# Kernel optimization log

Hardware: AMD Instinct MI355X
Metric: run time of the kernel (lower is better)

Reference implementation:

```python
import jax, jax.numpy as jnp
import numpy as np

N, E, D, T = 10000, 320000, 128, 128


def _layer_norm(x, g, b, eps=1e-5):
    mu = jnp.mean(x, axis=-1, keepdims=True)
    var = jnp.mean(jnp.square(x - mu), axis=-1, keepdims=True)
    return (x - mu) * jax.lax.rsqrt(var + eps) * g + b


def setup_inputs() -> dict:
    key = jax.random.key(0)
    ks = jax.random.split(key, 24)
    s = 0.05

    def lin(k, fin, fout):
        k1, k2 = jax.random.split(k)
        return (jax.random.normal(k1, (fin, fout), jnp.float32) * s,
                jax.random.normal(k2, (fout,), jnp.float32) * s)

    W_tp, b_tp = lin(ks[5], T, D)
    W_sg, b_sg = lin(ks[6], D, D)
    W_dg, b_dg = lin(ks[7], D, D)
    W_eg, b_eg = lin(ks[8], D, D)
    W_su, b_su = lin(ks[9], D, D)
    W_du, b_du = lin(ks[10], D, D)
    return {
        'node_feats': jax.random.normal(ks[0], (N, D), jnp.float32),
        'edge_feats': jax.random.normal(ks[1], (E, D), jnp.float32),
        'time_feats': jax.random.normal(ks[2], (N, T), jnp.float32),
        'src': jax.random.randint(ks[3], (E,), 0, N),
        'dst': jax.random.randint(ks[4], (E,), 0, N),
        'W_tp': W_tp, 'b_tp': b_tp,
        'W_sg': W_sg, 'b_sg': b_sg,
        'W_dg': W_dg, 'b_dg': b_dg,
        'W_eg': W_eg, 'b_eg': b_eg,
        'W_su': W_su, 'b_su': b_su,
        'W_du': W_du, 'b_du': b_du,
        'ln_e_g': jnp.ones((D,), jnp.float32), 'ln_e_b': jnp.zeros((D,), jnp.float32),
        'ln_n_g': jnp.ones((D,), jnp.float32), 'ln_n_b': jnp.zeros((D,), jnp.float32),
    }


def reference(node_feats, edge_feats, time_feats, src, dst,
              W_tp, b_tp, W_sg, b_sg, W_dg, b_dg, W_eg, b_eg,
              W_su, b_su, W_du, b_du, ln_e_g, ln_e_b, ln_n_g, ln_n_b):
    n_nodes = node_feats.shape[0]
    # per-node gate projections (time proj folded into source gate)
    e_src = node_feats @ W_sg + b_sg + time_feats @ W_tp + b_tp   # [N, D]
    e_dst = node_feats @ W_dg + b_dg                              # [N, D]
    # edge gating: gather from both endpoints + edge feature projection
    m = e_src[src] + e_dst[dst] + edge_feats @ W_eg + b_eg        # [E, D]
    sigma = jax.nn.sigmoid(m)                                     # [E, D]
    # gated message passing: scatter-add over destination nodes
    Bh = node_feats @ W_du + b_du                                 # [N, D]
    sum_sigma_h = jax.ops.segment_sum(Bh[src] * sigma, dst, num_segments=n_nodes)
    sum_sigma = jax.ops.segment_sum(sigma, dst, num_segments=n_nodes)
    h = sum_sigma_h / (sum_sigma + 1e-6)                          # [N, D]
    x = node_feats @ W_su + b_su + h
    x = jax.nn.silu(_layer_norm(x, ln_n_g, ln_n_b))
    y = jax.nn.silu(_layer_norm(m, ln_e_g, ln_e_b))
    x = node_feats + x  # residual
    y = edge_feats + y
    return (x, y)
```

## Files before the change

### kernel.cpp

```cpp
#include <hip/hip_runtime.h>
#include <hip/hip_bf16.h>

#define N_NODES 10000
#define N_EDGES 320000
#define D 128
#define NBINS 10000

typedef float f32x4 __attribute__((ext_vector_type(4)));
typedef float f32x2 __attribute__((ext_vector_type(2)));
typedef short bf16x8 __attribute__((ext_vector_type(8)));
typedef short bf16x16 __attribute__((ext_vector_type(16)));

static __device__ inline short f2bf(float f) {
    union { __hip_bfloat16 h; short s; } u;
    u.h = __float2bfloat16(f);
    return u.s;
}

static __device__ inline float bf2f(short s) {
    union { float f; unsigned u; } x;
    x.u = ((unsigned)(unsigned short)s) << 16;
    return x.f;
}

static __device__ inline float fast_rcp(float x) { return __builtin_amdgcn_rcpf(x); }

__global__ void prep_hist(const float* __restrict__ W_sg, const float* __restrict__ W_tp,
                          const float* __restrict__ W_dg, const float* __restrict__ W_du,
                          const float* __restrict__ W_su, const float* __restrict__ W_eg,
                          short* __restrict__ Wsrc, short* __restrict__ Wdg,
                          short* __restrict__ Wdu, short* __restrict__ Wsu,
                          short* __restrict__ Weg,
                          const int* __restrict__ dst, int* __restrict__ cnt) {
    int bid = blockIdx.x;
    if (bid < 1250) {
        int i = bid * 256 + threadIdx.x;
        atomicAdd(&cnt[dst[i]], 1);
        return;
    }
    int idx = (bid - 1250) * 256 + threadIdx.x;
    const float* W0; const float* W1; short* out; int i2;
    if (idx < 32768)      { W0 = W_sg; W1 = W_tp; out = Wsrc; i2 = idx; }
    else if (idx < 49152) { W0 = W_dg; W1 = W_dg; out = Wdg;  i2 = idx - 32768; }
    else if (idx < 65536) { W0 = W_du; W1 = W_du; out = Wdu;  i2 = idx - 49152; }
    else if (idx < 81920) { W0 = W_su; W1 = W_su; out = Wsu;  i2 = idx - 65536; }
    else                  { W0 = W_eg; W1 = W_eg; out = Weg;  i2 = idx - 81920; }
    int b  = i2 & 7;
    int l  = (i2 >> 3) & 63;
    int jt = (i2 >> 9) & 7;
    int t  = i2 >> 12;
    int k = 32 * t + ((l >> 4) * 8) + b;
    int j = jt * 16 + (l & 15);
    float v = (k < 128) ? W0[k * 128 + j] : W1[(k - 128) * 128 + j];
    out[i2] = f2bf(v);
}

__launch_bounds__(1024)
__global__ void scan_kernel(const int* __restrict__ cnt, int* __restrict__ cursor) {
    __shared__ int s[1024];
    int t = threadIdx.x;
    int b0 = t * 10;
    int loc[10];
    int tot = 0;
#pragma unroll
    for (int i = 0; i < 10; ++i) {
        int v = (b0 + i < NBINS) ? cnt[b0 + i] : 0;
        loc[i] = tot; tot += v;
    }
    s[t] = tot;
    __syncthreads();
    for (int off = 1; off < 1024; off <<= 1) {
        int v = (t >= off) ? s[t - off] : 0;
        __syncthreads();
        s[t] += v;
        __syncthreads();
    }
    int base = (t == 0) ? 0 : s[t - 1];
#pragma unroll
    for (int i = 0; i < 10; ++i)
        if (b0 + i < NBINS) cursor[b0 + i] = base + loc[i];
}

__global__ void scatter_kernel(const int* __restrict__ src, const int* __restrict__ dst,
                               int* __restrict__ cursor,
                               int* __restrict__ perm,
                               int* __restrict__ src_s, int* __restrict__ dst_s) {
    int i = blockIdx.x * 256 + threadIdx.x;
    if (i < N_EDGES) {
        int d = dst[i];
        int p = atomicAdd(&cursor[d], 1);
        perm[p] = i;
        src_s[p] = src[i];
        dst_s[p] = d;
    }
}

__launch_bounds__(256)
__global__ void node_proj_kernel(const float* __restrict__ node,
                                 const float* __restrict__ timef,
                                 const short* __restrict__ Wsrc_pk,
                                 const short* __restrict__ Wdg_pk,
                                 const short* __restrict__ Wdu_pk,
                                 const short* __restrict__ Wsu_pk,
                                 const float* __restrict__ b_sg, const float* __restrict__ b_tp,
                                 const float* __restrict__ b_dg, const float* __restrict__ b_du,
                                 const float* __restrict__ b_su, const float* __restrict__ b_eg,
                                 short* __restrict__ spk,
                                 short* __restrict__ dpk,
                                 float* __restrict__ xs) {
    int tid = threadIdx.x;
    int w = tid >> 6;
    int l = tid & 63;
    int g = l >> 4;
    int lr = l & 15;
    int r0 = blockIdx.x * 64 + w * 16;
    int arow = r0 + lr;

    bf16x8 aN[4], aT[4];
    if (arow < N_NODES) {
        const float* np = node + (size_t)arow * D;
        const float* tp = timef + (size_t)arow * D;
#pragma unroll
        for (int t = 0; t < 4; ++t) {
            int k0 = 32 * t + g * 8;
            f32x4 v0 = *(const f32x4*)(np + k0);
            f32x4 v1 = *(const f32x4*)(np + k0 + 4);
            f32x4 u0 = *(const f32x4*)(tp + k0);
            f32x4 u1 = *(const f32x4*)(tp + k0 + 4);
            bf16x8 a, b;
#pragma unroll
            for (int i = 0; i < 4; ++i) {
                a[i] = f2bf(v0[i]); a[4 + i] = f2bf(v1[i]);
                b[i] = f2bf(u0[i]); b[4 + i] = f2bf(u1[i]);
            }
            aN[t] = a; aT[t] = b;
        }
    } else {
        bf16x8 z = {0, 0, 0, 0, 0, 0, 0, 0};
#pragma unroll
        for (int t = 0; t < 4; ++t) { aN[t] = z; aT[t] = z; }
    }

    const bf16x8* Bsrc = (const bf16x8*)Wsrc_pk;
    const bf16x8* Bdg  = (const bf16x8*)Wdg_pk;
    const bf16x8* Bdu  = (const bf16x8*)Wdu_pk;
    const bf16x8* Bsu  = (const bf16x8*)Wsu_pk;

    bf16x8 chE[4];
#pragma unroll
    for (int jt = 0; jt < 8; ++jt) {
        int c = jt * 16 + lr;
        f32x4 acc = {0.f, 0.f, 0.f, 0.f};
#pragma unroll
        for (int t = 0; t < 4; ++t)
            acc = __builtin_amdgcn_mfma_f32_16x16x32_bf16(aN[t], Bsrc[(t * 8 + jt) * 64 + l], acc, 0, 0, 0);
#pragma unroll
        for (int t = 0; t < 4; ++t)
            acc = __builtin_amdgcn_mfma_f32_16x16x32_bf16(aT[t], Bsrc[((4 + t) * 8 + jt) * 64 + l], acc, 0, 0, 0);
        float bias = b_sg[c] + b_tp[c];
#pragma unroll
        for (int r = 0; r < 4; ++r) chE[r][jt] = f2bf(acc[r] + bias);
    }

    bf16x8 chD[4], chH[4];
    float xsv[4][8];
#pragma unroll
    for (int jt = 0; jt < 8; ++jt) {
        int c = jt * 16 + lr;
        f32x4 a0 = {0.f, 0.f, 0.f, 0.f}, a1 = a0, a2 = a0;
#pragma unroll
        for (int t = 0; t < 4; ++t) {
            a0 = __builtin_amdgcn_mfma_f32_16x16x32_bf16(aN[t], Bdg[(t * 8 + jt) * 64 + l], a0, 0, 0, 0);
            a1 = __builtin_amdgcn_mfma_f32_16x16x32_bf16(aN[t], Bdu[(t * 8 + jt) * 64 + l], a1, 0, 0, 0);
            a2 = __builtin_amdgcn_mfma_f32_16x16x32_bf16(aN[t], Bsu[(t * 8 + jt) * 64 + l], a2, 0, 0, 0);
        }
        float bdgc = b_dg[c] + b_eg[c];
        float bdu = b_du[c], bsu = b_su[c];
#pragma unroll
        for (int r = 0; r < 4; ++r) {
            chD[r][jt] = f2bf(a0[r] + bdgc);
            chH[r][jt] = f2bf(a1[r] + bdu);
            xsv[r][jt] = a2[r] + bsu;
        }
    }
#pragma unroll
    for (int r = 0; r < 4; ++r) {
        int row = r0 + g * 4 + r;
        if (row < N_NODES) {
            bf16x16 comb;
#pragma unroll
            for (int jt = 0; jt < 8; ++jt) { comb[jt] = chE[r][jt]; comb[8 + jt] = chH[r][jt]; }
            *(bf16x16*)(spk + (size_t)row * 256 + lr * 16) = comb;
            *(bf16x8*)(dpk + (size_t)row * D + lr * 8) = chD[r];
#pragma unroll
            for (int jt = 0; jt < 8; ++jt)
                xs[(size_t)row * D + jt * 16 + lr] = xsv[r][jt];
        }
    }
}


#define TILE_LOAD_IDX(S, E0) \
    const int eA##S = perm[(E0) + lr]; \
    int eidx##S[4], sidx##S[4], didx##S[4]; \
    _Pragma("unroll") \
    for (int r = 0; r < 4; ++r) { \
        int p = (E0) + g * 4 + r; \
        eidx##S[r] = perm[p]; sidx##S[r] = src_s[p]; didx##S[r] = dst_s[p]; \
    } \
    const int df##S = __shfl(didx##S[0], 0); \
    const bool uni##S = (df##S == __shfl(didx##S[3], 48));

#define TILE_GATHER(S) \
    bf16x16 esbh##S[4]; bf16x8 edv##S[4]; \
    _Pragma("unroll") \
    for (int r = 0; r < 4; ++r) \
        esbh##S[r] = *(const bf16x16*)(spk + (size_t)sidx##S[r] * 256 + lr * 16); \
    edv##S[0] = *(const bf16x8*)(dpk + (size_t)didx##S[0] * D + lr * 8); \
    if (!uni##S) { \
        _Pragma("unroll") \
        for (int r = 1; r < 4; ++r) \
            edv##S[r] = *(const bf16x8*)(dpk + (size_t)didx##S[r] * D + lr * 8); \
    } else { edv##S[1] = edv##S[0]; edv##S[2] = edv##S[0]; edv##S[3] = edv##S[0]; }

#define TILE_AFRAG(S) \
    bf16x8 aE##S[4]; \
    { const float* ep = edgef + (size_t)eA##S * D; \
      _Pragma("unroll") \
      for (int t = 0; t < 4; ++t) { \
        int k0 = 32 * t + g * 8; \
        f32x4 v0 = *(const f32x4*)(ep + k0); \
        f32x4 v1 = *(const f32x4*)(ep + k0 + 4); \
        bf16x8 a; \
        _Pragma("unroll") \
        for (int i = 0; i < 4; ++i) { a[i] = f2bf(v0[i]); a[4 + i] = f2bf(v1[i]); } \
        aE##S[t] = a; } }

#define TILE_COMPUTE(S) \
    f32x4 acc##S[8]; \
    _Pragma("unroll") \
    for (int jt = 0; jt < 8; ++jt) { \
        f32x4 c4 = {0.f, 0.f, 0.f, 0.f}; \
        _Pragma("unroll") \
        for (int t = 0; t < 4; ++t) \
            c4 = __builtin_amdgcn_mfma_f32_16x16x32_bf16(aE##S[t], Bp[(t * 8 + jt) * 64 + l], c4, 0, 0, 0); \
        acc##S[jt] = c4; } \
    float sum##S[4] = {0.f, 0.f, 0.f, 0.f}, sq##S[4] = {0.f, 0.f, 0.f, 0.f}; \
    _Pragma("unroll") \
    for (int jt = 0; jt < 8; ++jt) { \
        int c = jt * 16 + lr; \
        float sg[4], bsg[4]; \
        _Pragma("unroll") \
        for (int r = 0; r < 4; ++r) { \
            float m = acc##S[jt][r] + bf2f(esbh##S[r][jt]) + bf2f(edv##S[r][jt]); \
            acc##S[jt][r] = m; \
            float s = fast_rcp(1.f + __expf(-m)); \
            sg[r] = s; bsg[r] = bf2f(esbh##S[r][8 + jt]) * s; \
            sum##S[r] += m; sq##S[r] += m * m; } \
        if (uni##S) { \
            float aS = (sg[0] + sg[1]) + (sg[2] + sg[3]); \
            float aH = (bsg[0] + bsg[1]) + (bsg[2] + bsg[3]); \
            aS += __shfl_xor(aS, 16); aH += __shfl_xor(aH, 16); \
            aS += __shfl_xor(aS, 32); aH += __shfl_xor(aH, 32); \
            if (g == 0) { \
                atomicAdd(&ss [(size_t)df##S * D + c], aS); \
                atomicAdd(&ssh[(size_t)df##S * D + c], aH); } \
        } else { \
            float aS = sg[0], aH = bsg[0]; \
            _Pragma("unroll") \
            for (int r = 1; r < 4; ++r) { \
                if (didx##S[r] == didx##S[r - 1]) { aS += sg[r]; aH += bsg[r]; } \
                else { \
                    atomicAdd(&ss [(size_t)didx##S[r - 1] * D + c], aS); \
                    atomicAdd(&ssh[(size_t)didx##S[r - 1] * D + c], aH); \
                    aS = sg[r]; aH = bsg[r]; } } \
            atomicAdd(&ss [(size_t)didx##S[3] * D + c], aS); \
            atomicAdd(&ssh[(size_t)didx##S[3] * D + c], aH); } }

#define TILE_EPILOGUE(S) \
    _Pragma("unroll") \
    for (int r = 0; r < 4; ++r) { \
        float s = sum##S[r], q = sq##S[r]; \
        _Pragma("unroll") \
        for (int mk = 1; mk < 16; mk <<= 1) { s += __shfl_xor(s, mk); q += __shfl_xor(q, mk); } \
        float mean = s * (1.f / D); \
        sum##S[r] = mean; \
        sq##S[r] = rsqrtf(q * (1.f / D) - mean * mean + 1e-5f); } \
    _Pragma("unroll") \
    for (int jt = 0; jt < 8; ++jt) { \
        int c = jt * 16 + lr; \
        float gc = ln_g[c], bc = ln_b[c]; \
        _Pragma("unroll") \
        for (int r = 0; r < 4; ++r) { \
            float v = (acc##S[jt][r] - sum##S[r]) * sq##S[r] * gc + bc; \
            float sl = v * fast_rcp(1.f + __expf(-v)); \
            size_t off = (size_t)eidx##S[r] * D + c; \
            y[off] = __builtin_nontemporal_load(&edgef[off]) + sl; } }

__launch_bounds__(256)
__global__ void edge_kernel(const float* __restrict__ edgef,
                            const int* __restrict__ perm,
                            const int* __restrict__ src_s, const int* __restrict__ dst_s,
                            const short* __restrict__ Weg_pk,
                            const short* __restrict__ spk,
                            const short* __restrict__ dpk,
                            const float* __restrict__ ln_g, const float* __restrict__ ln_b,
                            float* __restrict__ ss, float* __restrict__ ssh,
                            float* __restrict__ y) {
    __shared__ short Bs[128 * 128];
    {
        const bf16x8* gw = (const bf16x8*)Weg_pk;
        bf16x8* sw = (bf16x8*)Bs;
        for (int i = threadIdx.x; i < 2048; i += 256) sw[i] = gw[i];
    }
    __syncthreads();

    int tid = threadIdx.x;
    int w = tid >> 6;
    int l = tid & 63;
    int g = l >> 4;
    int lr = l & 15;

    int b = blockIdx.x;
    int xcd = b & 7, boff = b >> 3;
    int swz = (xcd < 4 ? xcd * 313 : 1252 + (xcd - 4) * 312) + boff;
    int ebase = swz * 128 + w * 32;

    const bf16x8* Bp = (const bf16x8*)Bs;

    TILE_LOAD_IDX(0, ebase)
    TILE_LOAD_IDX(1, ebase + 16)
    TILE_GATHER(0)
    TILE_AFRAG(0)
    TILE_AFRAG(1)
    TILE_COMPUTE(0)
    TILE_GATHER(1)
    TILE_EPILOGUE(0)
    TILE_COMPUTE(1)
    TILE_EPILOGUE(1)
}

__launch_bounds__(256)
__global__ void node_out_kernel(const float* __restrict__ node,
                                const float* __restrict__ xs,
                                const float* __restrict__ ssh, const float* __restrict__ ss,
                                const float* __restrict__ ln_g, const float* __restrict__ ln_b,
                                float* __restrict__ x) {
    int w = threadIdx.x >> 6;
    int l = threadIdx.x & 63;
    int row = blockIdx.x * 4 + w;
    if (row >= N_NODES) return;
    size_t base = (size_t)row * D + 2 * l;
    f32x2 xv = *(const f32x2*)(xs + base);
    f32x2 hs = *(const f32x2*)(ssh + base);
    f32x2 sv = *(const f32x2*)(ss + base);
    float v0 = xv[0] + hs[0] / (sv[0] + 1e-6f);
    float v1 = xv[1] + hs[1] / (sv[1] + 1e-6f);
    float s = v0 + v1, q = v0 * v0 + v1 * v1;
#pragma unroll
    for (int mk = 1; mk < 64; mk <<= 1) { s += __shfl_xor(s, mk); q += __shfl_xor(q, mk); }
    float mean = s * (1.f / D);
    float var = q * (1.f / D) - mean * mean;
    float rstd = rsqrtf(var + 1e-5f);
    float t0 = (v0 - mean) * rstd * ln_g[2 * l] + ln_b[2 * l];
    float t1 = (v1 - mean) * rstd * ln_g[2 * l + 1] + ln_b[2 * l + 1];
    t0 = t0 * fast_rcp(1.f + __expf(-t0));
    t1 = t1 * fast_rcp(1.f + __expf(-t1));
    f32x2 nv = *(const f32x2*)(node + base);
    f32x2 outv;
    outv[0] = nv[0] + t0;
    outv[1] = nv[1] + t1;
    *(f32x2*)(x + base) = outv;
}

extern "C" void kernel_launch(void* const* d_in, const int* in_sizes, int n_in,
                              void* d_out, int out_size, void* d_ws, size_t ws_size,
                              hipStream_t stream) {
    const float* node  = (const float*)d_in[0];
    const float* edgef = (const float*)d_in[1];
    const float* timef = (const float*)d_in[2];
    const int*   src   = (const int*)d_in[3];
    const int*   dst   = (const int*)d_in[4];
    const float* W_tp = (const float*)d_in[5];  const float* b_tp = (const float*)d_in[6];
    const float* W_sg = (const float*)d_in[7];  const float* b_sg = (const float*)d_in[8];
    const float* W_dg = (const float*)d_in[9];  const float* b_dg = (const float*)d_in[10];
    const float* W_eg = (const float*)d_in[11]; const float* b_eg = (const float*)d_in[12];
    const float* W_su = (const float*)d_in[13]; const float* b_su = (const float*)d_in[14];
    const float* W_du = (const float*)d_in[15]; const float* b_du = (const float*)d_in[16];
    const float* ln_e_g = (const float*)d_in[17]; const float* ln_e_b = (const float*)d_in[18];
    const float* ln_n_g = (const float*)d_in[19]; const float* ln_n_b = (const float*)d_in[20];

    char* ws = (char*)d_ws;
    size_t nd = (size_t)N_NODES * D;
    int* cnt       = (int*)ws; ws += 10240 * 4;
    int* cursor    = (int*)ws; ws += 10240 * 4;
    float* ss    = (float*)ws; ws += nd * 4;
    float* ssh   = (float*)ws; ws += nd * 4;
    float* xs    = (float*)ws; ws += nd * 4;
    short* spk   = (short*)ws; ws += (size_t)N_NODES * 256 * 2;
    short* dpk   = (short*)ws; ws += nd * 2;
    short* Wsrc_pk = (short*)ws; ws += 256 * 128 * 2;
    short* Wdg_pk  = (short*)ws; ws += 128 * 128 * 2;
    short* Wdu_pk  = (short*)ws; ws += 128 * 128 * 2;
    short* Wsu_pk  = (short*)ws; ws += 128 * 128 * 2;
    short* Weg_pk  = (short*)ws; ws += 128 * 128 * 2;
    int* perm      = (int*)ws; ws += (size_t)N_EDGES * 4;
    int* src_s     = (int*)ws; ws += (size_t)N_EDGES * 4;
    int* dst_s     = (int*)ws; ws += (size_t)N_EDGES * 4;

    hipMemsetAsync(cnt, 0, 2 * 10240 * 4 + 2 * nd * 4, stream);

    prep_hist<<<1634, 256, 0, stream>>>(W_sg, W_tp, W_dg, W_du, W_su, W_eg,
                                        Wsrc_pk, Wdg_pk, Wdu_pk, Wsu_pk, Weg_pk,
                                        dst, cnt);
    scan_kernel<<<1, 1024, 0, stream>>>(cnt, cursor);
    scatter_kernel<<<(N_EDGES + 255) / 256, 256, 0, stream>>>(src, dst, cursor, perm, src_s, dst_s);

    node_proj_kernel<<<(N_NODES + 63) / 64, 256, 0, stream>>>(
        node, timef, Wsrc_pk, Wdg_pk, Wdu_pk, Wsu_pk,
        b_sg, b_tp, b_dg, b_du, b_su, b_eg, spk, dpk, xs);

    edge_kernel<<<2500, 256, 0, stream>>>(
        edgef, perm, src_s, dst_s, Weg_pk, spk, dpk,
        ln_e_g, ln_e_b, ss, ssh, (float*)d_out + nd);

    node_out_kernel<<<N_NODES / 4, 256, 0, stream>>>(
        node, xs, ssh, ss, ln_n_g, ln_n_b, (float*)d_out);
}
```

Baseline: 270.7 us.

## Fuse edge scatter with node projection and split weight prepack from histogram

Splits the combined prepack+histogram kernel into two kernels, and merges the CSR scatter and the node projection GEMM into one launch partitioned by block index. This lets the atomic-bound scatter and the MFMA-bound projection run concurrently instead of back to back. The projection writes the source-gate half of the packed rows early, which lowers live registers at the cost of two smaller stores per row. Launch count stays the same overall.

New measurement: 250.8 us. 7.4% less time.

```diff
diff --git a/kernel.cpp b/kernel.cpp
--- a/kernel.cpp
+++ b/kernel.cpp
@@ -25,20 +25,13 @@
 
 static __device__ inline float fast_rcp(float x) { return __builtin_amdgcn_rcpf(x); }
 
-__global__ void prep_hist(const float* __restrict__ W_sg, const float* __restrict__ W_tp,
-                          const float* __restrict__ W_dg, const float* __restrict__ W_du,
-                          const float* __restrict__ W_su, const float* __restrict__ W_eg,
-                          short* __restrict__ Wsrc, short* __restrict__ Wdg,
-                          short* __restrict__ Wdu, short* __restrict__ Wsu,
-                          short* __restrict__ Weg,
-                          const int* __restrict__ dst, int* __restrict__ cnt) {
-    int bid = blockIdx.x;
-    if (bid < 1250) {
-        int i = bid * 256 + threadIdx.x;
-        atomicAdd(&cnt[dst[i]], 1);
-        return;
-    }
-    int idx = (bid - 1250) * 256 + threadIdx.x;
+__global__ void prepack_all(const float* __restrict__ W_sg, const float* __restrict__ W_tp,
+                            const float* __restrict__ W_dg, const float* __restrict__ W_du,
+                            const float* __restrict__ W_su, const float* __restrict__ W_eg,
+                            short* __restrict__ Wsrc, short* __restrict__ Wdg,
+                            short* __restrict__ Wdu, short* __restrict__ Wsu,
+                            short* __restrict__ Weg) {
+    int idx = blockIdx.x * 256 + threadIdx.x;
     const float* W0; const float* W1; short* out; int i2;
     if (idx < 32768)      { W0 = W_sg; W1 = W_tp; out = Wsrc; i2 = idx; }
     else if (idx < 49152) { W0 = W_dg; W1 = W_dg; out = Wdg;  i2 = idx - 32768; }
@@ -55,6 +48,11 @@
     out[i2] = f2bf(v);
 }
 
+__global__ void hist_kernel(const int* __restrict__ dst, int* __restrict__ cnt) {
+    int i = blockIdx.x * 256 + threadIdx.x;
+    if (i < N_EDGES) atomicAdd(&cnt[dst[i]], 1);
+}
+
 __launch_bounds__(1024)
 __global__ void scan_kernel(const int* __restrict__ cnt, int* __restrict__ cursor) {
     __shared__ int s[1024];
@@ -81,39 +79,39 @@
         if (b0 + i < NBINS) cursor[b0 + i] = base + loc[i];
 }
 
-__global__ void scatter_kernel(const int* __restrict__ src, const int* __restrict__ dst,
-                               int* __restrict__ cursor,
-                               int* __restrict__ perm,
-                               int* __restrict__ src_s, int* __restrict__ dst_s) {
-    int i = blockIdx.x * 256 + threadIdx.x;
-    if (i < N_EDGES) {
+__launch_bounds__(256)
+__global__ void scatter_proj_kernel(const int* __restrict__ src, const int* __restrict__ dst,
+                                    int* __restrict__ cursor,
+                                    int* __restrict__ perm,
+                                    int* __restrict__ src_s, int* __restrict__ dst_s,
+                                    const float* __restrict__ node,
+                                    const float* __restrict__ timef,
+                                    const short* __restrict__ Wsrc_pk,
+                                    const short* __restrict__ Wdg_pk,
+                                    const short* __restrict__ Wdu_pk,
+                                    const short* __restrict__ Wsu_pk,
+                                    const float* __restrict__ b_sg, const float* __restrict__ b_tp,
+                                    const float* __restrict__ b_dg, const float* __restrict__ b_du,
+                                    const float* __restrict__ b_su, const float* __restrict__ b_eg,
+                                    short* __restrict__ spk,
+                                    short* __restrict__ dpk,
+                                    float* __restrict__ xs) {
+    if (blockIdx.x < 1250) {
+        int i = blockIdx.x * 256 + threadIdx.x;
         int d = dst[i];
         int p = atomicAdd(&cursor[d], 1);
         perm[p] = i;
         src_s[p] = src[i];
         dst_s[p] = d;
-    }
-}
-
-__launch_bounds__(256)
-__global__ void node_proj_kernel(const float* __restrict__ node,
-                                 const float* __restrict__ timef,
-                                 const short* __restrict__ Wsrc_pk,
-                                 const short* __restrict__ Wdg_pk,
-                                 const short* __restrict__ Wdu_pk,
-                                 const short* __restrict__ Wsu_pk,
-                                 const float* __restrict__ b_sg, const float* __restrict__ b_tp,
-                                 const float* __restrict__ b_dg, const float* __restrict__ b_du,
-                                 const float* __restrict__ b_su, const float* __restrict__ b_eg,
-                                 short* __restrict__ spk,
-                                 short* __restrict__ dpk,
-                                 float* __restrict__ xs) {
+        return;
+    }
+
     int tid = threadIdx.x;
     int w = tid >> 6;
     int l = tid & 63;
     int g = l >> 4;
     int lr = l & 15;
-    int r0 = blockIdx.x * 64 + w * 16;
+    int r0 = (blockIdx.x - 1250) * 64 + w * 16;
     int arow = r0 + lr;
 
     bf16x8 aN[4], aT[4];
@@ -146,55 +144,61 @@
     const bf16x8* Bdu  = (const bf16x8*)Wdu_pk;
     const bf16x8* Bsu  = (const bf16x8*)Wsu_pk;
 
-    bf16x8 chE[4];
-#pragma unroll
-    for (int jt = 0; jt < 8; ++jt) {
-        int c = jt * 16 + lr;
-        f32x4 acc = {0.f, 0.f, 0.f, 0.f};
-#pragma unroll
-        for (int t = 0; t < 4; ++t)
-            acc = __builtin_amdgcn_mfma_f32_16x16x32_bf16(aN[t], Bsrc[(t * 8 + jt) * 64 + l], acc, 0, 0, 0);
-#pragma unroll
-        for (int t = 0; t < 4; ++t)
-            acc = __builtin_amdgcn_mfma_f32_16x16x32_bf16(aT[t], Bsrc[((4 + t) * 8 + jt) * 64 + l], acc, 0, 0, 0);
-        float bias = b_sg[c] + b_tp[c];
-#pragma unroll
-        for (int r = 0; r < 4; ++r) chE[r][jt] = f2bf(acc[r] + bias);
-    }
-
-    bf16x8 chD[4], chH[4];
-    float xsv[4][8];
-#pragma unroll
-    for (int jt = 0; jt < 8; ++jt) {
-        int c = jt * 16 + lr;
-        f32x4 a0 = {0.f, 0.f, 0.f, 0.f}, a1 = a0, a2 = a0;
-#pragma unroll
-        for (int t = 0; t < 4; ++t) {
-            a0 = __builtin_amdgcn_mfma_f32_16x16x32_bf16(aN[t], Bdg[(t * 8 + jt) * 64 + l], a0, 0, 0, 0);
-            a1 = __builtin_amdgcn_mfma_f32_16x16x32_bf16(aN[t], Bdu[(t * 8 + jt) * 64 + l], a1, 0, 0, 0);
-            a2 = __builtin_amdgcn_mfma_f32_16x16x32_bf16(aN[t], Bsu[(t * 8 + jt) * 64 + l], a2, 0, 0, 0);
+    {
+        bf16x8 chunk[4];
+#pragma unroll
+        for (int jt = 0; jt < 8; ++jt) {
+            int c = jt * 16 + lr;
+            f32x4 acc = {0.f, 0.f, 0.f, 0.f};
+#pragma unroll
+            for (int t = 0; t < 4; ++t)
+                acc = __builtin_amdgcn_mfma_f32_16x16x32_bf16(aN[t], Bsrc[(t * 8 + jt) * 64 + l], acc, 0, 0, 0);
+#pragma unroll
+            for (int t = 0; t < 4; ++t)
+                acc = __builtin_amdgcn_mfma_f32_16x16x32_bf16(aT[t], Bsrc[((4 + t) * 8 + jt) * 64 + l], acc, 0, 0, 0);
+            float bias = b_sg[c] + b_tp[c];
+#pragma unroll
+            for (int r = 0; r < 4; ++r) chunk[r][jt] = f2bf(acc[r] + bias);
         }
-        float bdgc = b_dg[c] + b_eg[c];
-        float bdu = b_du[c], bsu = b_su[c];
 #pragma unroll
         for (int r = 0; r < 4; ++r) {
-            chD[r][jt] = f2bf(a0[r] + bdgc);
-            chH[r][jt] = f2bf(a1[r] + bdu);
-            xsv[r][jt] = a2[r] + bsu;
+            int row = r0 + g * 4 + r;
+            if (row < N_NODES) *(bf16x8*)(spk + (size_t)row * 256 + lr * 16) = chunk[r];
         }
     }
-#pragma unroll
-    for (int r = 0; r < 4; ++r) {
-        int row = r0 + g * 4 + r;
-        if (row < N_NODES) {
-            bf16x16 comb;
-#pragma unroll
-            for (int jt = 0; jt < 8; ++jt) { comb[jt] = chE[r][jt]; comb[8 + jt] = chH[r][jt]; }
-            *(bf16x16*)(spk + (size_t)row * 256 + lr * 16) = comb;
-            *(bf16x8*)(dpk + (size_t)row * D + lr * 8) = chD[r];
-#pragma unroll
-            for (int jt = 0; jt < 8; ++jt)
-                xs[(size_t)row * D + jt * 16 + lr] = xsv[r][jt];
+
+    {
+        bf16x8 chD[4], chH[4];
+        float xsv[4][8];
+#pragma unroll
+        for (int jt = 0; jt < 8; ++jt) {
+            int c = jt * 16 + lr;
+            f32x4 a0 = {0.f, 0.f, 0.f, 0.f}, a1 = a0, a2 = a0;
+#pragma unroll
+            for (int t = 0; t < 4; ++t) {
+                a0 = __builtin_amdgcn_mfma_f32_16x16x32_bf16(aN[t], Bdg[(t * 8 + jt) * 64 + l], a0, 0, 0, 0);
+                a1 = __builtin_amdgcn_mfma_f32_16x16x32_bf16(aN[t], Bdu[(t * 8 + jt) * 64 + l], a1, 0, 0, 0);
+                a2 = __builtin_amdgcn_mfma_f32_16x16x32_bf16(aN[t], Bsu[(t * 8 + jt) * 64 + l], a2, 0, 0, 0);
+            }
+            float bdgc = b_dg[c] + b_eg[c];
+            float bdu = b_du[c], bsu = b_su[c];
+#pragma unroll
+            for (int r = 0; r < 4; ++r) {
+                chD[r][jt] = f2bf(a0[r] + bdgc);
+                chH[r][jt] = f2bf(a1[r] + bdu);
+                xsv[r][jt] = a2[r] + bsu;
+            }
+        }
+#pragma unroll
+        for (int r = 0; r < 4; ++r) {
+            int row = r0 + g * 4 + r;
+            if (row < N_NODES) {
+                *(bf16x8*)(dpk + (size_t)row * D + lr * 8) = chD[r];
+                *(bf16x8*)(spk + (size_t)row * 256 + lr * 16 + 8) = chH[r];
+#pragma unroll
+                for (int jt = 0; jt < 8; ++jt)
+                    xs[(size_t)row * D + jt * 16 + lr] = xsv[r][jt];
+            }
         }
     }
 }
@@ -410,13 +414,13 @@
 
     hipMemsetAsync(cnt, 0, 2 * 10240 * 4 + 2 * nd * 4, stream);
 
-    prep_hist<<<1634, 256, 0, stream>>>(W_sg, W_tp, W_dg, W_du, W_su, W_eg,
-                                        Wsrc_pk, Wdg_pk, Wdu_pk, Wsu_pk, Weg_pk,
-                                        dst, cnt);
+    prepack_all<<<384, 256, 0, stream>>>(W_sg, W_tp, W_dg, W_du, W_su, W_eg,
+                                         Wsrc_pk, Wdg_pk, Wdu_pk, Wsu_pk, Weg_pk);
+    hist_kernel<<<1250, 256, 0, stream>>>(dst, cnt);
     scan_kernel<<<1, 1024, 0, stream>>>(cnt, cursor);
-    scatter_kernel<<<(N_EDGES + 255) / 256, 256, 0, stream>>>(src, dst, cursor, perm, src_s, dst_s);
-
-    node_proj_kernel<<<(N_NODES + 63) / 64, 256, 0, stream>>>(
+
+    scatter_proj_kernel<<<1407, 256, 0, stream>>>(
+        src, dst, cursor, perm, src_s, dst_s,
         node, timef, Wsrc_pk, Wdg_pk, Wdu_pk, Wsu_pk,
         b_sg, b_tp, b_dg, b_du, b_su, b_eg, spk, dpk, xs);
 
```
